# Optimization experiments

Hardware: AMD Instinct MI355X
Metric: run time of the kernel (lower is better)

The kernel has to match this reference:

```python
import jax, jax.numpy as jnp
import numpy as np
from jax import lax

D = 768
C = 37          # num_classes + 1
PAD_ID = C - 1  # label_init puts '[PAD]' last
B, S = 128, 512


def setup_inputs() -> dict:
    key = jax.random.key(0)
    ks = jax.random.split(key, 8)
    x = jax.random.normal(ks[0], (B, S, D), dtype=jnp.float32)
    W = jax.random.normal(ks[1], (D, C), dtype=jnp.float32) * (1.0 / np.sqrt(D))
    b = jnp.zeros((C,), dtype=jnp.float32)
    start = jax.random.uniform(ks[2], (C,), minval=-0.1, maxval=0.1)
    end = jax.random.uniform(ks[3], (C,), minval=-0.1, maxval=0.1)
    trans = jax.random.uniform(ks[4], (C, C), minval=-0.1, maxval=0.1)
    labels = jax.random.randint(ks[5], (B, S), 0, C)
    lengths = jax.random.randint(ks[6], (B,), 16, S + 1)
    mask = (jnp.arange(S)[None, :] < lengths[:, None])  # first column always True
    return {"x": x, "W": W, "b": b, "start": start, "end": end,
            "trans": trans, "labels": labels, "mask": mask}


def _crf(emissions, labels, mask, start, end, trans):
    # time-major, as in pytorch-crf
    em = jnp.transpose(emissions, (1, 0, 2))      # [S, B, C]
    tg = labels.T                                  # [S, B]
    mkb = mask.T                                   # [S, B] bool
    mkf = mkb.astype(em.dtype)
    bidx = jnp.arange(em.shape[1])

    # ---- gold path score ----
    score0 = start[tg[0]] + em[0, bidx, tg[0]]
    def step_score(carry, inp):
        prev_tag, s = carry
        e_t, t_t, mf, mb = inp
        s = s + (trans[prev_tag, t_t] + e_t[bidx, t_t]) * mf
        prev_tag = jnp.where(mb, t_t, prev_tag)
        return (prev_tag, s), None
    (last_tag, score), _ = lax.scan(step_score, (tg[0], score0),
                                    (em[1:], tg[1:], mkf[1:], mkb[1:]))
    score = score + end[last_tag]

    # ---- log partition (forward algorithm) ----
    alpha0 = start[None, :] + em[0]               # [B, C]
    def step_norm(alpha, inp):
        e_t, mb = inp
        nxt = jax.nn.logsumexp(alpha[:, :, None] + trans[None, :, :], axis=1) + e_t
        return jnp.where(mb[:, None], nxt, alpha), None
    alpha, _ = lax.scan(step_norm, alpha0, (em[1:], mkb[1:]))
    logZ = jax.nn.logsumexp(alpha + end[None, :], axis=1)
    ll = jnp.sum(score - logZ)                    # reduction='sum'

    # ---- Viterbi decode ----
    ident = jnp.arange(C)[None, :]
    v0 = start[None, :] + em[0]
    def step_vit(v, inp):
        e_t, mb = inp
        cand = v[:, :, None] + trans[None, :, :]  # [B, prev, cur]
        bp = jnp.argmax(cand, axis=1)             # [B, C]
        nxt = jnp.max(cand, axis=1) + e_t
        v = jnp.where(mb[:, None], nxt, v)
        bp = jnp.where(mb[:, None], bp, ident)    # identity at padded steps
        return v, bp
    v, bps = lax.scan(step_vit, v0, (em[1:], mkb[1:]))  # bps: [S-1, B, C]
    last = jnp.argmax(v + end[None, :], axis=1)   # [B]
    def back(tag, bp):
        return bp[bidx, tag], tag
    first, rest = lax.scan(back, last, bps, reverse=True)
    tags = jnp.concatenate([first[None, :], rest], axis=0).T  # [B, S]
    tags = jnp.where(mask, tags, PAD_ID)
    return ll, tags


def reference(x, W, b, start, end, trans, labels, mask):
    emissions = jnp.einsum('bsd,dc->bsc', x, W) + b  # linear head
    log_likelihood, tags = _crf(emissions, labels, mask, start, end, trans)
    return log_likelihood, tags
```

## Files before the change

### kernel.cpp

```cpp
#include <hip/hip_runtime.h>

#define Bq 128
#define Sq 512
#define Cq 37
#define Dq 768

typedef __attribute__((ext_vector_type(2))) float f32x2;
typedef __attribute__((ext_vector_type(4))) float f32x4;
typedef __attribute__((ext_vector_type(8))) short bf16x8;

static __device__ __forceinline__ f32x2 pk_fma(f32x2 a, f32x2 b, f32x2 c) {
  f32x2 d; asm("v_pk_fma_f32 %0, %1, %2, %3" : "=v"(d) : "v"(a), "v"(b), "v"(c));
  return d;
}
static __device__ __forceinline__ f32x2 pk_add(f32x2 a, f32x2 b) {
  f32x2 d; asm("v_pk_add_f32 %0, %1, %2" : "=v"(d) : "v"(a), "v"(b));
  return d;
}
static __device__ __forceinline__ float bcast(float v, int p) {
  return __int_as_float(__builtin_amdgcn_ds_bpermute(p << 2, __float_as_int(v)));
}

#define REP18(X) X(0)X(1)X(2)X(3)X(4)X(5)X(6)X(7)X(8)X(9)X(10)X(11)X(12)X(13) \
  X(14)X(15)X(16)X(17)
#define REP37(X) X(0)X(1)X(2)X(3)X(4)X(5)X(6)X(7)X(8)X(9)X(10)X(11)X(12)X(13) \
  X(14)X(15)X(16)X(17)X(18)X(19)X(20)X(21)X(22)X(23)X(24)X(25)X(26)X(27)X(28) \
  X(29)X(30)X(31)X(32)X(33)X(34)X(35)X(36)

__global__ __launch_bounds__(256) void prep_kernel(
    const float* __restrict__ W, unsigned short* __restrict__ Wbh,
    unsigned short* __restrict__ Wbl)
{
  int i = blockIdx.x * 256 + threadIdx.x;
  if (i >= 24 * 3 * 64 * 8) return;
  int ks = i / 1536, rem = i % 1536;
  int nt = rem / 512, rem2 = rem % 512;
  int lane = rem2 >> 3, j = rem2 & 7;
  int k = ks * 32 + (lane >> 4) * 8 + j;
  int c = nt * 16 + (lane & 15);
  float w = (c < Cq) ? W[(size_t)k * Cq + c] : 0.f;
  unsigned u = __float_as_uint(w);
  unsigned short h = (unsigned short)(u >> 16);
  float hr = __uint_as_float((unsigned)h << 16);
  float r = w - hr;
  Wbh[i] = h;
  Wbl[i] = (unsigned short)(__float_as_uint(r) >> 16);
}

__global__ __launch_bounds__(256) void emis_kernel(
    const float* __restrict__ x, const unsigned short* __restrict__ Wbh,
    const unsigned short* __restrict__ Wbl, const float* __restrict__ bias,
    float* __restrict__ em)
{
  int tid = threadIdx.x, lane = tid & 63;
  int wv = tid >> 6;
  int tokBase = blockIdx.x * 64 + wv * 16;
  int row = lane & 15, kg = lane >> 4;
  const float* xr = x + (size_t)(tokBase + row) * Dq + kg * 8;
  const bf16x8* Bh = (const bf16x8*)Wbh;
  const bf16x8* Bl = (const bf16x8*)Wbl;
  f32x4 acc0 = {0.f, 0.f, 0.f, 0.f};
  f32x4 acc1 = {0.f, 0.f, 0.f, 0.f};
  f32x4 acc2 = {0.f, 0.f, 0.f, 0.f};

  float4 c0 = *(const float4*)(xr);
  float4 c1 = *(const float4*)(xr + 4);
  for (int ks = 0; ks < 24; ++ks) {
    float4 n0, n1;
    if (ks < 23) {
      n0 = *(const float4*)(xr + (ks + 1) * 32);
      n1 = *(const float4*)(xr + (ks + 1) * 32 + 4);
    }
    bf16x8 ah, al;
#define SPLIT(J, V) { unsigned u = __float_as_uint(V); \
    unsigned short h = (unsigned short)(u >> 16); \
    float hr = __uint_as_float((unsigned)h << 16); \
    float rr = (V) - hr; \
    ah[J] = (short)h; al[J] = (short)(__float_as_uint(rr) >> 16); }
    SPLIT(0, c0.x) SPLIT(1, c0.y) SPLIT(2, c0.z) SPLIT(3, c0.w)
    SPLIT(4, c1.x) SPLIT(5, c1.y) SPLIT(6, c1.z) SPLIT(7, c1.w)
#undef SPLIT
    int fi = (ks * 3) * 64 + lane;
    bf16x8 bh0 = Bh[fi], bh1 = Bh[fi + 64], bh2 = Bh[fi + 128];
    bf16x8 bl0 = Bl[fi], bl1 = Bl[fi + 64], bl2 = Bl[fi + 128];
    acc0 = __builtin_amdgcn_mfma_f32_16x16x32_bf16(al, bh0, acc0, 0, 0, 0);
    acc1 = __builtin_amdgcn_mfma_f32_16x16x32_bf16(al, bh1, acc1, 0, 0, 0);
    acc2 = __builtin_amdgcn_mfma_f32_16x16x32_bf16(al, bh2, acc2, 0, 0, 0);
    acc0 = __builtin_amdgcn_mfma_f32_16x16x32_bf16(ah, bl0, acc0, 0, 0, 0);
    acc1 = __builtin_amdgcn_mfma_f32_16x16x32_bf16(ah, bl1, acc1, 0, 0, 0);
    acc2 = __builtin_amdgcn_mfma_f32_16x16x32_bf16(ah, bl2, acc2, 0, 0, 0);
    acc0 = __builtin_amdgcn_mfma_f32_16x16x32_bf16(ah, bh0, acc0, 0, 0, 0);
    acc1 = __builtin_amdgcn_mfma_f32_16x16x32_bf16(ah, bh1, acc1, 0, 0, 0);
    acc2 = __builtin_amdgcn_mfma_f32_16x16x32_bf16(ah, bh2, acc2, 0, 0, 0);
    c0 = n0; c1 = n1;
  }
  int colc = lane & 15;
#pragma unroll
  for (int r = 0; r < 4; ++r) {
    size_t tok = (size_t)tokBase + kg * 4 + r;
    em[tok * Cq + colc]      = acc0[r] + bias[colc];
    em[tok * Cq + 16 + colc] = acc1[r] + bias[16 + colc];
    if (colc < 5)
      em[tok * Cq + 32 + colc] = acc2[r] + bias[32 + colc];
  }
}

__global__ __launch_bounds__(320) void crf_mega_kernel(
    const float* __restrict__ em, const float* __restrict__ startv,
    const float* __restrict__ endv, const float* __restrict__ trans,
    const int* __restrict__ labels, const unsigned char* __restrict__ maskb,
    float* __restrict__ llp, float* __restrict__ outp)
{
  __shared__ float semm[(Sq + 4) * Cq];
  __shared__ float vh[Sq * 40];
  __shared__ __align__(16) float sxA[64];
  __shared__ __align__(16) float sxB[64];
  __shared__ __align__(16) float sxC[64];
  __shared__ __align__(16) float sxD[64];
  __shared__ float mrgA[64], mrgB[64], mrgV[64], mrgU[64];
  __shared__ float s_score;
  __shared__ int s_cstar;
  int b = blockIdx.x;
  int tid = threadIdx.x, wid = tid >> 6, lane = tid & 63;
  int cl = lane < Cq ? lane : Cq - 1;

  int esz4 = (maskb[1] == 0) ? 1 : 0;
  int len = 0;
#pragma unroll
  for (int k = 0; k < 8; ++k) {
    size_t t = (size_t)lane + (size_t)k * 64;
    unsigned char mb = esz4 ? maskb[((size_t)b * Sq + t) * 4] : maskb[(size_t)b * Sq + t];
    len += (mb != 0);
  }
#pragma unroll
  for (int off = 32; off; off >>= 1) len += __shfl_xor(len, off);
  int m = len >> 1;

  const float4* src4 = (const float4*)(em + (size_t)b * Sq * Cq);
  float4* dst4 = (float4*)semm;
  for (int i = tid; i < (Sq * Cq) / 4; i += 320) dst4[i] = src4[i];
  if (tid < 4 * Cq) semm[Sq * Cq + tid] = 0.f;
  __syncthreads();

  const float L2E = 1.4426950408889634f, LN2 = 0.6931471805599453f;

  if (wid == 0) {
    f32x2 E2[18];
#pragma unroll
    for (int i = 0; i < 18; ++i) {
      E2[i][0] = exp2f(trans[(2 * i) * Cq + cl] * L2E);
      E2[i][1] = exp2f(trans[(2 * i + 1) * Cq + cl] * L2E);
    }
    float E36 = exp2f(trans[36 * Cq + cl] * L2E);
    const float4* se4 = (const float4*)sxA;
    float a0 = (lane < Cq) ? (startv[cl] + semm[cl]) : -3.0e38f;
    float K0 = bcast(a0, 0);
    float ez = (lane < Cq) ? exp2f((a0 - K0) * L2E) : 0.f;
    int eacc = 0;
    float wA = exp2f(semm[1 * Cq + cl] * L2E), wB = exp2f(semm[2 * Cq + cl] * L2E);
    float wC = exp2f(semm[3 * Cq + cl] * L2E), wD = exp2f(semm[4 * Cq + cl] * L2E);
    for (int t = 1; t <= m; ++t) {
      sxA[lane] = ez;
      int tn = (t + 4 <= m) ? t + 4 : m;
      float raw = semm[tn * Cq + cl];
      float4 gv[10];
#pragma unroll
      for (int q = 0; q < 10; ++q) gv[q] = se4[q];
      int e0 = ((__float_as_int(gv[0].x) >> 23) & 255) - 127;
      float scale = __int_as_float((127 - e0) << 23);
      f32x2 sa = {0.f, 0.f}, sb2 = {0.f, 0.f};
#define FPK(i) { f32x2 g; \
      g[0] = ((i) & 1) ? gv[(i) >> 1].z : gv[(i) >> 1].x; \
      g[1] = ((i) & 1) ? gv[(i) >> 1].w : gv[(i) >> 1].y; \
      if ((i) & 1) sb2 = pk_fma(g, E2[i], sb2); else sa = pk_fma(g, E2[i], sa); }
      REP18(FPK)
#undef FPK
      float dot = ((sa[0] + sb2[0]) + (sa[1] + sb2[1])) + gv[9].x * E36;
      float wcur = wA; wA = wB; wB = wC; wC = wD;
      ez = dot * (wcur * scale);
      eacc += e0;
      wD = exp2f(raw * L2E);
    }
    mrgA[lane] = (lane < Cq) ? LN2 * (log2f(ez) + (float)eacc) + K0 : -3.0e38f;
  } else if (wid == 1) {
    f32x2 E2[18];
#pragma unroll
    for (int i = 0; i < 18; ++i) {
      E2[i][0] = exp2f(trans[cl * Cq + 2 * i] * L2E);
      E2[i][1] = exp2f(trans[cl * Cq + 2 * i + 1] * L2E);
    }
    float E36 = exp2f(trans[cl * Cq + 36] * L2E);
    const float4* se4 = (const float4*)sxB;
    float b0v = (lane < Cq) ? endv[cl] : -3.0e38f;
    float KB = bcast(b0v, 0);
    float bz = (lane < Cq) ? exp2f((b0v - KB) * L2E) : 0.f;
    int eacc = 0;
    float wA = exp2f(semm[(len - 1) * Cq + cl] * L2E);
    float wB = exp2f(semm[(len - 2) * Cq + cl] * L2E);
    float wC = exp2f(semm[(len - 3) * Cq + cl] * L2E);
    float wD = exp2f(semm[(len - 4) * Cq + cl] * L2E);
    for (int t = len - 2; t >= m; --t) {
      float wcur = wA; wA = wB; wB = wC; wC = wD;
      float s = bz * wcur;
      sxB[lane] = s;
      int tn = (t - 3 > 0) ? t - 3 : 0;
      float raw = semm[tn * Cq + cl];
      float4 gv[10];
#pragma unroll
      for (int q = 0; q < 10; ++q) gv[q] = se4[q];
      int e0 = ((__float_as_int(gv[0].x) >> 23) & 255) - 127;
      float scale = __int_as_float((127 - e0) << 23);
      f32x2 sa = {0.f, 0.f}, sb2 = {0.f, 0.f};
#define FPK(i) { f32x2 g; \
      g[0] = ((i) & 1) ? gv[(i) >> 1].z : gv[(i) >> 1].x; \
      g[1] = ((i) & 1) ? gv[(i) >> 1].w : gv[(i) >> 1].y; \
      if ((i) & 1) sb2 = pk_fma(g, E2[i], sb2); else sa = pk_fma(g, E2[i], sa); }
      REP18(FPK)
#undef FPK
      float dot = ((sa[0] + sb2[0]) + (sa[1] + sb2[1])) + gv[9].x * E36;
      bz = dot * scale;
      eacc += e0;
      wD = exp2f(raw * L2E);
    }
    mrgB[lane] = (lane < Cq) ? LN2 * (log2f(bz) + (float)eacc) + KB : -3.0e38f;
  } else if (wid == 2) {
    f32x2 T2[18];
#pragma unroll
    for (int i = 0; i < 18; ++i) {
      T2[i][0] = trans[(2 * i) * Cq + cl];
      T2[i][1] = trans[(2 * i + 1) * Cq + cl];
    }
    float T36 = trans[36 * Cq + cl];
    const float4* sv4 = (const float4*)sxC;
    float v = (lane < Cq) ? (startv[cl] + semm[cl]) : -3.0e38f;
    vh[0 * 40 + lane] = (lane < Cq) ? v : -3.0e38f;
    float emA = semm[1 * Cq + cl], emB = semm[2 * Cq + cl];
    float emC = semm[3 * Cq + cl], emD = semm[4 * Cq + cl];
    for (int t = 1; t <= m; ++t) {
      sxC[lane] = v;
      int tn = (t + 4 <= m) ? t + 4 : m;
      float raw = semm[tn * Cq + cl];
      float4 gv[10];
#pragma unroll
      for (int q = 0; q < 10; ++q) gv[q] = sv4[q];
      float m0 = -3.0e38f, m1 = -3.0e38f, m2 = -3.0e38f, m3 = -3.0e38f;
#define VPK(i) { f32x2 g; \
      g[0] = ((i) & 1) ? gv[(i) >> 1].z : gv[(i) >> 1].x; \
      g[1] = ((i) & 1) ? gv[(i) >> 1].w : gv[(i) >> 1].y; \
      f32x2 c = pk_add(g, T2[i]); \
      if (((i) & 3) == 0) m0 = fmaxf(fmaxf(m0, c[0]), c[1]); \
      else if (((i) & 3) == 1) m1 = fmaxf(fmaxf(m1, c[0]), c[1]); \
      else if (((i) & 3) == 2) m2 = fmaxf(fmaxf(m2, c[0]), c[1]); \
      else m3 = fmaxf(fmaxf(m3, c[0]), c[1]); }
      REP18(VPK)
#undef VPK
      float c36 = gv[9].x + T36;
      float best = fmaxf(fmaxf(fmaxf(m0, m1), fmaxf(m2, m3)), c36);
      float emc = emA; emA = emB; emB = emC; emC = emD;
      v = (lane < Cq) ? best + emc : -3.0e38f;
      vh[t * 40 + lane] = v;
      emD = raw;
    }
    mrgV[lane] = v;
  } else if (wid == 3) {
    f32x2 T2[18];
#pragma unroll
    for (int i = 0; i < 18; ++i) {
      T2[i][0] = trans[cl * Cq + 2 * i];
      T2[i][1] = trans[cl * Cq + 2 * i + 1];
    }
    float T36 = trans[cl * Cq + 36];
    const float4* sv4 = (const float4*)sxD;
    float u = (lane < Cq) ? endv[cl] : -3.0e38f;
    float emA = semm[(len - 1) * Cq + cl], emB = semm[(len - 2) * Cq + cl];
    float emC = semm[(len - 3) * Cq + cl], emD = semm[(len - 4) * Cq + cl];
    for (int t = len - 2; t >= m; --t) {
      float emc = emA; emA = emB; emB = emC; emC = emD;
      float s = u + emc;
      sxD[lane] = s;
      vh[(t + 1) * 40 + lane] = (lane < Cq) ? s : -3.0e38f;
      int tn = (t - 3 > 0) ? t - 3 : 0;
      float raw = semm[tn * Cq + cl];
      float4 gv[10];
#pragma unroll
      for (int q = 0; q < 10; ++q) gv[q] = sv4[q];
      float m0 = -3.0e38f, m1 = -3.0e38f, m2 = -3.0e38f, m3 = -3.0e38f;
#define VPK(i) { f32x2 g; \
      g[0] = ((i) & 1) ? gv[(i) >> 1].z : gv[(i) >> 1].x; \
      g[1] = ((i) & 1) ? gv[(i) >> 1].w : gv[(i) >> 1].y; \
      f32x2 c = pk_add(g, T2[i]); \
      if (((i) & 3) == 0) m0 = fmaxf(fmaxf(m0, c[0]), c[1]); \
      else if (((i) & 3) == 1) m1 = fmaxf(fmaxf(m1, c[0]), c[1]); \
      else if (((i) & 3) == 2) m2 = fmaxf(fmaxf(m2, c[0]), c[1]); \
      else m3 = fmaxf(fmaxf(m3, c[0]), c[1]); }
      REP18(VPK)
#undef VPK
      float c36 = gv[9].x + T36;
      float best = fmaxf(fmaxf(fmaxf(m0, m1), fmaxf(m2, m3)), c36);
      u = (lane < Cq) ? best : -3.0e38f;
      emD = raw;
    }
    mrgU[lane] = u;
  } else {
    const int* lab = labels + (size_t)b * Sq;
    float sc = 0.f;
#pragma unroll
    for (int k = 0; k < 8; ++k) {
      int t = 1 + lane + k * 64;
      if (t < len) {
        int lp = lab[t - 1], lt = lab[t];
        sc += trans[lp * Cq + lt] + semm[t * Cq + lt];
      }
    }
#pragma unroll
    for (int off = 32; off; off >>= 1) sc += __shfl_xor(sc, off);
    if (lane == 0) {
      int l0 = lab[0], lf = lab[len - 1];
      s_score = sc + startv[l0] + semm[l0] + endv[lf];
    }
  }
  __syncthreads();

  unsigned char* bpl = (unsigned char*)semm;
  if (wid == 0) {
    float xv = (lane < Cq) ? mrgA[lane] + mrgB[lane] : -3.0e38f;
    float mm = xv;
#pragma unroll
    for (int off = 32; off; off >>= 1) mm = fmaxf(mm, __shfl_xor(mm, off));
    float es = exp2f((xv - mm) * L2E);
#pragma unroll
    for (int off = 32; off; off >>= 1) es += __shfl_xor(es, off);
    float logZ = mm + log2f(es) * LN2;
    float pv = (lane < Cq) ? mrgV[lane] + mrgU[lane] : -3.0e38f;
    int idx = (lane < Cq) ? lane : 1000;
#pragma unroll
    for (int off = 32; off; off >>= 1) {
      float po = __shfl_xor(pv, off); int io = __shfl_xor(idx, off);
      if (po > pv || (po == pv && io < idx)) { pv = po; idx = io; }
    }
    if (lane == 0) { llp[b] = s_score - logZ; s_cstar = idx; }
  } else if (wid <= 2) {
#define DECLT(i) float T##i = trans[(i) * Cq + cl];
    REP37(DECLT)
#undef DECLT
    for (int t = wid; t <= m; t += 2) {
      const float4* vr4 = (const float4*)&vh[(t - 1) * 40];
      float4 gv[10];
#pragma unroll
      for (int q = 0; q < 10; ++q) gv[q] = vr4[q];
      float br[40]; float4* br4 = (float4*)br;
#pragma unroll
      for (int q = 0; q < 10; ++q) br4[q] = gv[q];
      float best = -3.0e38f; int bi = 0;
#define BARG(i) { float cnd = br[i] + T##i; if (cnd > best) { best = cnd; bi = (i); } }
      REP37(BARG)
#undef BARG
      if (lane < Cq) bpl[cl * 520 + t] = (unsigned char)bi;
    }
  } else {
#define DECLR(i) float R##i = trans[cl * Cq + (i)];
    REP37(DECLR)
#undef DECLR
    for (int s = m + 1 + (wid - 3); s < len; s += 2) {
      const float4* vr4 = (const float4*)&vh[s * 40];
      float4 gv[10];
#pragma unroll
      for (int q = 0; q < 10; ++q) gv[q] = vr4[q];
      float br[40]; float4* br4 = (float4*)br;
#pragma unroll
      for (int q = 0; q < 10; ++q) br4[q] = gv[q];
      float best = -3.0e38f; int bi = 0;
#define BARG(i) { float cnd = br[i] + R##i; if (cnd > best) { best = cnd; bi = (i); } }
      REP37(BARG)
#undef BARG
      if (lane < Cq) bpl[cl * 520 + s] = (unsigned char)bi;
    }
  }
  __syncthreads();

  if (wid == 0) {
    int cstar = __builtin_amdgcn_readfirstlane(s_cstar);
    int lenv = __builtin_amdgcn_readfirstlane(len);
    int mv = __builtin_amdgcn_readfirstlane(m);
    int rowc = lane < Cq ? lane : Cq - 1;
    const unsigned* rw = (const unsigned*)(bpl + rowc * 520);
    unsigned r[128];
#pragma unroll
    for (int k = 0; k < 128; ++k) r[k] = rw[k];
    unsigned vt[8];
#pragma unroll
    for (int j = 0; j < 8; ++j) vt[j] = 0u;
#pragma unroll
    for (int j = 0; j < 8; ++j)
      vt[j] = (lane == (mv & 63) && (mv >> 6) == j) ? (unsigned)cstar : vt[j];
    {
      int tag = cstar;
#pragma unroll
      for (int t = 1; t <= 510; ++t) {
        int word = __builtin_amdgcn_readlane((int)r[t >> 2], tag);
        int nt = (word >> ((t & 3) * 8)) & 0xff;
        bool live = (t > mv) && (t < lenv);
        tag = live ? nt : tag;
        vt[t >> 6] = (lane == (t & 63) && live) ? (unsigned)tag : vt[t >> 6];
      }
    }
    {
      int tag = cstar;
#pragma unroll
      for (int t = 510; t >= 0; --t) {
        int word = __builtin_amdgcn_readlane((int)r[(t + 1) >> 2], tag);
        int nt = (word >> (((t + 1) & 3) * 8)) & 0xff;
        bool live = (t + 1 <= mv);
        tag = live ? nt : tag;
        vt[t >> 6] = (lane == (t & 63) && live) ? (unsigned)tag : vt[t >> 6];
      }
    }
#pragma unroll
    for (int j = 0; j < 8; ++j) {
      int t = j * 64 + lane;
      float o = (t < lenv) ? (float)(int)vt[j] : 36.0f;
      outp[(size_t)b * Sq + t] = o;
    }
  }
}

__global__ __launch_bounds__(64) void ll_reduce_kernel(
    const float* __restrict__ llp, float* __restrict__ outp)
{
  int lane = threadIdx.x;
  float s = llp[lane] + llp[lane + 64];
#pragma unroll
  for (int off = 32; off; off >>= 1) s += __shfl_xor(s, off);
  if (lane == 0) outp[0] = s;
}

extern "C" void kernel_launch(void* const* d_in, const int* in_sizes, int n_in,
                              void* d_out, int out_size, void* d_ws, size_t ws_size,
                              hipStream_t stream)
{
  const float* x      = (const float*)d_in[0];
  const float* W      = (const float*)d_in[1];
  const float* bias   = (const float*)d_in[2];
  const float* startv = (const float*)d_in[3];
  const float* endv   = (const float*)d_in[4];
  const float* trans  = (const float*)d_in[5];
  const int*   labels = (const int*)d_in[6];
  const unsigned char* maskb = (const unsigned char*)d_in[7];
  float* out = (float*)d_out;

  char* ws = (char*)d_ws;
  float* em            = (float*)(ws);
  float* llp           = (float*)(ws + 9699328);
  unsigned short* Wbh  = (unsigned short*)(ws + 9699840);
  unsigned short* Wbl  = (unsigned short*)(ws + 9773568);

  prep_kernel<<<144, 256, 0, stream>>>(W, Wbh, Wbl);
  emis_kernel<<<1024, 256, 0, stream>>>(x, Wbh, Wbl, bias, em);
  crf_mega_kernel<<<128, 320, 0, stream>>>(em, startv, endv, trans, labels, maskb,
                                           llp, out + 1);
  ll_reduce_kernel<<<1, 64, 0, stream>>>(llp, out);
}
```

Measured before the change: 187.3 us.

## Balance backpointer argmax across all waves and split traceback into two waves

The backpointer computation, previously split between two fixed wave pairs (forward and backward halves), now runs on all five waves with interleaved rows. Each argmax is done as a tree-based max followed by a min-index reduction instead of a serial compare chain. The forward and backward Viterbi traceback chains move onto separate waves so they run concurrently, and each wave writes only its own part of the output. The intent is to shorten the serial tail of the decode phase. The cost is higher register pressure from holding both transition vectors and all candidates, and tie-breaking now relies on exact equality with the max.

```diff
diff --git a/kernel.cpp b/kernel.cpp
--- a/kernel.cpp
+++ b/kernel.cpp
@@ -20,12 +20,16 @@
 static __device__ __forceinline__ float bcast(float v, int p) {
   return __int_as_float(__builtin_amdgcn_ds_bpermute(p << 2, __float_as_int(v)));
 }
+static __device__ __forceinline__ int imin(int a, int b) { return a < b ? a : b; }
 
 #define REP18(X) X(0)X(1)X(2)X(3)X(4)X(5)X(6)X(7)X(8)X(9)X(10)X(11)X(12)X(13) \
   X(14)X(15)X(16)X(17)
 #define REP37(X) X(0)X(1)X(2)X(3)X(4)X(5)X(6)X(7)X(8)X(9)X(10)X(11)X(12)X(13) \
   X(14)X(15)X(16)X(17)X(18)X(19)X(20)X(21)X(22)X(23)X(24)X(25)X(26)X(27)X(28) \
   X(29)X(30)X(31)X(32)X(33)X(34)X(35)X(36)
+
+#define BR(i) ((((i) & 3) == 0) ? gv[(i) >> 2].x : (((i) & 3) == 1) ? gv[(i) >> 2].y \
+             : (((i) & 3) == 2) ? gv[(i) >> 2].z : gv[(i) >> 2].w)
 
 __global__ __launch_bounds__(256) void prep_kernel(
     const float* __restrict__ W, unsigned short* __restrict__ Wbh,
@@ -233,7 +237,7 @@
     float T36 = trans[36 * Cq + cl];
     const float4* sv4 = (const float4*)sxC;
     float v = (lane < Cq) ? (startv[cl] + semm[cl]) : -3.0e38f;
-    vh[0 * 40 + lane] = (lane < Cq) ? v : -3.0e38f;
+    if (lane < 40) vh[0 * 40 + lane] = v;
     float emA = semm[1 * Cq + cl], emB = semm[2 * Cq + cl];
     float emC = semm[3 * Cq + cl], emD = semm[4 * Cq + cl];
     for (int t = 1; t <= m; ++t) {
@@ -258,7 +262,7 @@
       float best = fmaxf(fmaxf(fmaxf(m0, m1), fmaxf(m2, m3)), c36);
       float emc = emA; emA = emB; emB = emC; emC = emD;
       v = (lane < Cq) ? best + emc : -3.0e38f;
-      vh[t * 40 + lane] = v;
+      if (lane < 40) vh[t * 40 + lane] = v;
       emD = raw;
     }
     mrgV[lane] = v;
@@ -278,7 +282,7 @@
       float emc = emA; emA = emB; emB = emC; emC = emD;
       float s = u + emc;
       sxD[lane] = s;
-      vh[(t + 1) * 40 + lane] = (lane < Cq) ? s : -3.0e38f;
+      if (lane < 40) vh[(t + 1) * 40 + lane] = (lane < Cq) ? s : -3.0e38f;
       int tn = (t - 3 > 0) ? t - 3 : 0;
       float raw = semm[tn * Cq + cl];
       float4 gv[10];
@@ -339,46 +343,78 @@
       if (po > pv || (po == pv && io < idx)) { pv = po; idx = io; }
     }
     if (lane == 0) { llp[b] = s_score - logZ; s_cstar = idx; }
-  } else if (wid <= 2) {
-#define DECLT(i) float T##i = trans[(i) * Cq + cl];
-    REP37(DECLT)
-#undef DECLT
-    for (int t = wid; t <= m; t += 2) {
-      const float4* vr4 = (const float4*)&vh[(t - 1) * 40];
+  }
+  {
+#define DT(i) float T##i = trans[(i) * Cq + cl];
+    REP37(DT)
+#undef DT
+#define DR(i) float R##i = trans[cl * Cq + (i)];
+    REP37(DR)
+#undef DR
+    for (int r = 1 + wid; r < len; r += 5) {
+      int isbp = (r <= m);
+      const float4* vr4 = (const float4*)&vh[(isbp ? r - 1 : r) * 40];
       float4 gv[10];
 #pragma unroll
       for (int q = 0; q < 10; ++q) gv[q] = vr4[q];
-      float br[40]; float4* br4 = (float4*)br;
-#pragma unroll
-      for (int q = 0; q < 10; ++q) br4[q] = gv[q];
-      float best = -3.0e38f; int bi = 0;
-#define BARG(i) { float cnd = br[i] + T##i; if (cnd > best) { best = cnd; bi = (i); } }
-      REP37(BARG)
-#undef BARG
-      if (lane < Cq) bpl[cl * 520 + t] = (unsigned char)bi;
-    }
-  } else {
-#define DECLR(i) float R##i = trans[cl * Cq + (i)];
-    REP37(DECLR)
-#undef DECLR
-    for (int s = m + 1 + (wid - 3); s < len; s += 2) {
-      const float4* vr4 = (const float4*)&vh[s * 40];
-      float4 gv[10];
-#pragma unroll
-      for (int q = 0; q < 10; ++q) gv[q] = vr4[q];
-      float br[40]; float4* br4 = (float4*)br;
-#pragma unroll
-      for (int q = 0; q < 10; ++q) br4[q] = gv[q];
-      float best = -3.0e38f; int bi = 0;
-#define BARG(i) { float cnd = br[i] + R##i; if (cnd > best) { best = cnd; bi = (i); } }
-      REP37(BARG)
-#undef BARG
-      if (lane < Cq) bpl[cl * 520 + s] = (unsigned char)bi;
+      int bi;
+      if (isbp) {
+#define CNDT(i) float C##i = BR(i) + T##i;
+        REP37(CNDT)
+#undef CNDT
+        float b0 = fmaxf(fmaxf(C0, C1), C2),   b1 = fmaxf(fmaxf(C3, C4), C5);
+        float b2 = fmaxf(fmaxf(C6, C7), C8),   b3 = fmaxf(fmaxf(C9, C10), C11);
+        float b4 = fmaxf(fmaxf(C12, C13), C14), b5 = fmaxf(fmaxf(C15, C16), C17);
+        float b6 = fmaxf(fmaxf(C18, C19), C20), b7 = fmaxf(fmaxf(C21, C22), C23);
+        float b8 = fmaxf(fmaxf(C24, C25), C26), b9 = fmaxf(fmaxf(C27, C28), C29);
+        float b10 = fmaxf(fmaxf(C30, C31), C32), b11 = fmaxf(fmaxf(C33, C34), C35);
+        float c0 = fmaxf(fmaxf(b0, b1), b2), c1 = fmaxf(fmaxf(b3, b4), b5);
+        float c2 = fmaxf(fmaxf(b6, b7), b8), c3 = fmaxf(fmaxf(b9, b10), b11);
+        float best = fmaxf(fmaxf(fmaxf(c0, c1), fmaxf(c2, c3)), C36);
+#define IDX(i) int I##i = (C##i == best) ? (i) : 63;
+        REP37(IDX)
+#undef IDX
+        int d0 = imin(imin(I0, I1), I2),   d1 = imin(imin(I3, I4), I5);
+        int d2 = imin(imin(I6, I7), I8),   d3 = imin(imin(I9, I10), I11);
+        int d4 = imin(imin(I12, I13), I14), d5 = imin(imin(I15, I16), I17);
+        int d6 = imin(imin(I18, I19), I20), d7 = imin(imin(I21, I22), I23);
+        int d8 = imin(imin(I24, I25), I26), d9 = imin(imin(I27, I28), I29);
+        int d10 = imin(imin(I30, I31), I32), d11 = imin(imin(I33, I34), I35);
+        int e0i = imin(imin(d0, d1), d2), e1i = imin(imin(d3, d4), d5);
+        int e2i = imin(imin(d6, d7), d8), e3i = imin(imin(d9, d10), d11);
+        bi = imin(imin(imin(e0i, e1i), imin(e2i, e3i)), I36);
+      } else {
+#define CNDR(i) float C##i = BR(i) + R##i;
+        REP37(CNDR)
+#undef CNDR
+        float b0 = fmaxf(fmaxf(C0, C1), C2),   b1 = fmaxf(fmaxf(C3, C4), C5);
+        float b2 = fmaxf(fmaxf(C6, C7), C8),   b3 = fmaxf(fmaxf(C9, C10), C11);
+        float b4 = fmaxf(fmaxf(C12, C13), C14), b5 = fmaxf(fmaxf(C15, C16), C17);
+        float b6 = fmaxf(fmaxf(C18, C19), C20), b7 = fmaxf(fmaxf(C21, C22), C23);
+        float b8 = fmaxf(fmaxf(C24, C25), C26), b9 = fmaxf(fmaxf(C27, C28), C29);
+        float b10 = fmaxf(fmaxf(C30, C31), C32), b11 = fmaxf(fmaxf(C33, C34), C35);
+        float c0 = fmaxf(fmaxf(b0, b1), b2), c1 = fmaxf(fmaxf(b3, b4), b5);
+        float c2 = fmaxf(fmaxf(b6, b7), b8), c3 = fmaxf(fmaxf(b9, b10), b11);
+        float best = fmaxf(fmaxf(fmaxf(c0, c1), fmaxf(c2, c3)), C36);
+#define IDX(i) int I##i = (C##i == best) ? (i) : 63;
+        REP37(IDX)
+#undef IDX
+        int d0 = imin(imin(I0, I1), I2),   d1 = imin(imin(I3, I4), I5);
+        int d2 = imin(imin(I6, I7), I8),   d3 = imin(imin(I9, I10), I11);
+        int d4 = imin(imin(I12, I13), I14), d5 = imin(imin(I15, I16), I17);
+        int d6 = imin(imin(I18, I19), I20), d7 = imin(imin(I21, I22), I23);
+        int d8 = imin(imin(I24, I25), I26), d9 = imin(imin(I27, I28), I29);
+        int d10 = imin(imin(I30, I31), I32), d11 = imin(imin(I33, I34), I35);
+        int e0i = imin(imin(d0, d1), d2), e1i = imin(imin(d3, d4), d5);
+        int e2i = imin(imin(d6, d7), d8), e3i = imin(imin(d9, d10), d11);
+        bi = imin(imin(imin(e0i, e1i), imin(e2i, e3i)), I36);
+      }
+      if (lane < Cq) bpl[cl * 520 + r] = (unsigned char)bi;
     }
   }
   __syncthreads();
 
-  if (wid == 0) {
+  if (wid <= 1) {
     int cstar = __builtin_amdgcn_readfirstlane(s_cstar);
     int lenv = __builtin_amdgcn_readfirstlane(len);
     int mv = __builtin_amdgcn_readfirstlane(m);
@@ -390,10 +426,25 @@
     unsigned vt[8];
 #pragma unroll
     for (int j = 0; j < 8; ++j) vt[j] = 0u;
-#pragma unroll
-    for (int j = 0; j < 8; ++j)
-      vt[j] = (lane == (mv & 63) && (mv >> 6) == j) ? (unsigned)cstar : vt[j];
-    {
+    if (wid == 0) {
+#pragma unroll
+      for (int j = 0; j < 8; ++j)
+        vt[j] = (lane == (mv & 63) && (mv >> 6) == j) ? (unsigned)cstar : vt[j];
+      int tag = cstar;
+#pragma unroll
+      for (int t = 510; t >= 0; --t) {
+        int word = __builtin_amdgcn_readlane((int)r[(t + 1) >> 2], tag);
+        int nt = (word >> (((t + 1) & 3) * 8)) & 0xff;
+        bool live = (t + 1 <= mv);
+        tag = live ? nt : tag;
+        vt[t >> 6] = (lane == (t & 63) && live) ? (unsigned)tag : vt[t >> 6];
+      }
+#pragma unroll
+      for (int j = 0; j < 8; ++j) {
+        int t = j * 64 + lane;
+        if (t <= mv) outp[(size_t)b * Sq + t] = (float)(int)vt[j];
+      }
+    } else {
       int tag = cstar;
 #pragma unroll
       for (int t = 1; t <= 510; ++t) {
@@ -403,23 +454,14 @@
         tag = live ? nt : tag;
         vt[t >> 6] = (lane == (t & 63) && live) ? (unsigned)tag : vt[t >> 6];
       }
-    }
-    {
-      int tag = cstar;
-#pragma unroll
-      for (int t = 510; t >= 0; --t) {
-        int word = __builtin_amdgcn_readlane((int)r[(t + 1) >> 2], tag);
-        int nt = (word >> (((t + 1) & 3) * 8)) & 0xff;
-        bool live = (t + 1 <= mv);
-        tag = live ? nt : tag;
-        vt[t >> 6] = (lane == (t & 63) && live) ? (unsigned)tag : vt[t >> 6];
+#pragma unroll
+      for (int j = 0; j < 8; ++j) {
+        int t = j * 64 + lane;
+        if (t > mv) {
+          float o = (t < lenv) ? (float)(int)vt[j] : 36.0f;
+          outp[(size_t)b * Sq + t] = o;
+        }
       }
-    }
-#pragma unroll
-    for (int j = 0; j < 8; ++j) {
-      int t = j * 64 + lane;
-      float o = (t < lenv) ? (float)(int)vt[j] : 36.0f;
-      outp[(size_t)b * Sq + t] = o;
     }
   }
 }
```

New measurement: 215.9 us. 15.3% more time.

## Split Viterbi backtrace across two waves and stream backpointer rows in chunks

Applied to the files above, without the earlier changes.

The backtrace previously ran serially in one wave, walking forward from the midpoint and then backward to the start. It now assigns each half to a separate wave so the two run concurrently. Each wave loads backpointer words in 16-word chunks instead of holding 128 registers, and uses ds_bpermute for the tag lookup in place of readlane. The change also drops the register copy into a br array in the argmax loops and limits vh stores to lanes below 40. Risks are the higher latency of bpermute on the dependent chain and the two waves writing disjoint output ranges.

```diff
diff --git a/kernel.cpp b/kernel.cpp
--- a/kernel.cpp
+++ b/kernel.cpp
@@ -26,6 +26,9 @@
 #define REP37(X) X(0)X(1)X(2)X(3)X(4)X(5)X(6)X(7)X(8)X(9)X(10)X(11)X(12)X(13) \
   X(14)X(15)X(16)X(17)X(18)X(19)X(20)X(21)X(22)X(23)X(24)X(25)X(26)X(27)X(28) \
   X(29)X(30)X(31)X(32)X(33)X(34)X(35)X(36)
+
+#define BR(i) ((((i) & 3) == 0) ? gv[(i) >> 2].x : (((i) & 3) == 1) ? gv[(i) >> 2].y \
+             : (((i) & 3) == 2) ? gv[(i) >> 2].z : gv[(i) >> 2].w)
 
 __global__ __launch_bounds__(256) void prep_kernel(
     const float* __restrict__ W, unsigned short* __restrict__ Wbh,
@@ -233,7 +236,7 @@
     float T36 = trans[36 * Cq + cl];
     const float4* sv4 = (const float4*)sxC;
     float v = (lane < Cq) ? (startv[cl] + semm[cl]) : -3.0e38f;
-    vh[0 * 40 + lane] = (lane < Cq) ? v : -3.0e38f;
+    if (lane < 40) vh[0 * 40 + lane] = v;
     float emA = semm[1 * Cq + cl], emB = semm[2 * Cq + cl];
     float emC = semm[3 * Cq + cl], emD = semm[4 * Cq + cl];
     for (int t = 1; t <= m; ++t) {
@@ -258,7 +261,7 @@
       float best = fmaxf(fmaxf(fmaxf(m0, m1), fmaxf(m2, m3)), c36);
       float emc = emA; emA = emB; emB = emC; emC = emD;
       v = (lane < Cq) ? best + emc : -3.0e38f;
-      vh[t * 40 + lane] = v;
+      if (lane < 40) vh[t * 40 + lane] = v;
       emD = raw;
     }
     mrgV[lane] = v;
@@ -278,7 +281,7 @@
       float emc = emA; emA = emB; emB = emC; emC = emD;
       float s = u + emc;
       sxD[lane] = s;
-      vh[(t + 1) * 40 + lane] = (lane < Cq) ? s : -3.0e38f;
+      if (lane < 40) vh[(t + 1) * 40 + lane] = (lane < Cq) ? s : -3.0e38f;
       int tn = (t - 3 > 0) ? t - 3 : 0;
       float raw = semm[tn * Cq + cl];
       float4 gv[10];
@@ -340,37 +343,31 @@
     }
     if (lane == 0) { llp[b] = s_score - logZ; s_cstar = idx; }
   } else if (wid <= 2) {
-#define DECLT(i) float T##i = trans[(i) * Cq + cl];
-    REP37(DECLT)
-#undef DECLT
+#define DT(i) float T##i = trans[(i) * Cq + cl];
+    REP37(DT)
+#undef DT
     for (int t = wid; t <= m; t += 2) {
       const float4* vr4 = (const float4*)&vh[(t - 1) * 40];
       float4 gv[10];
 #pragma unroll
       for (int q = 0; q < 10; ++q) gv[q] = vr4[q];
-      float br[40]; float4* br4 = (float4*)br;
-#pragma unroll
-      for (int q = 0; q < 10; ++q) br4[q] = gv[q];
       float best = -3.0e38f; int bi = 0;
-#define BARG(i) { float cnd = br[i] + T##i; if (cnd > best) { best = cnd; bi = (i); } }
+#define BARG(i) { float cnd = BR(i) + T##i; if (cnd > best) { best = cnd; bi = (i); } }
       REP37(BARG)
 #undef BARG
       if (lane < Cq) bpl[cl * 520 + t] = (unsigned char)bi;
     }
   } else {
-#define DECLR(i) float R##i = trans[cl * Cq + (i)];
-    REP37(DECLR)
-#undef DECLR
+#define DR(i) float R##i = trans[cl * Cq + (i)];
+    REP37(DR)
+#undef DR
     for (int s = m + 1 + (wid - 3); s < len; s += 2) {
       const float4* vr4 = (const float4*)&vh[s * 40];
       float4 gv[10];
 #pragma unroll
       for (int q = 0; q < 10; ++q) gv[q] = vr4[q];
-      float br[40]; float4* br4 = (float4*)br;
-#pragma unroll
-      for (int q = 0; q < 10; ++q) br4[q] = gv[q];
       float best = -3.0e38f; int bi = 0;
-#define BARG(i) { float cnd = br[i] + R##i; if (cnd > best) { best = cnd; bi = (i); } }
+#define BARG(i) { float cnd = BR(i) + R##i; if (cnd > best) { best = cnd; bi = (i); } }
       REP37(BARG)
 #undef BARG
       if (lane < Cq) bpl[cl * 520 + s] = (unsigned char)bi;
@@ -378,48 +375,67 @@
   }
   __syncthreads();
 
-  if (wid == 0) {
+  if (wid <= 1) {
     int cstar = __builtin_amdgcn_readfirstlane(s_cstar);
     int lenv = __builtin_amdgcn_readfirstlane(len);
     int mv = __builtin_amdgcn_readfirstlane(m);
     int rowc = lane < Cq ? lane : Cq - 1;
     const unsigned* rw = (const unsigned*)(bpl + rowc * 520);
-    unsigned r[128];
-#pragma unroll
-    for (int k = 0; k < 128; ++k) r[k] = rw[k];
     unsigned vt[8];
 #pragma unroll
     for (int j = 0; j < 8; ++j) vt[j] = 0u;
-#pragma unroll
-    for (int j = 0; j < 8; ++j)
-      vt[j] = (lane == (mv & 63) && (mv >> 6) == j) ? (unsigned)cstar : vt[j];
-    {
-      int tag = cstar;
-#pragma unroll
-      for (int t = 1; t <= 510; ++t) {
-        int word = __builtin_amdgcn_readlane((int)r[t >> 2], tag);
-        int nt = (word >> ((t & 3) * 8)) & 0xff;
-        bool live = (t > mv) && (t < lenv);
-        tag = live ? nt : tag;
-        vt[t >> 6] = (lane == (t & 63) && live) ? (unsigned)tag : vt[t >> 6];
+    int tag = cstar;
+    if (wid == 0) {
+#pragma unroll
+      for (int j = 0; j < 8; ++j)
+        vt[j] = (lane == (mv & 63) && (mv >> 6) == j) ? (unsigned)cstar : vt[j];
+#pragma unroll
+      for (int k = 7; k >= 0; --k) {
+        unsigned rc[16];
+#pragma unroll
+        for (int w = 0; w < 16; ++w) rc[w] = rw[16 * k + w];
+#pragma unroll
+        for (int tt = 63; tt >= 0; --tt) {
+          int p = 64 * k + tt;
+          if (p == 0) continue;
+          int t = p - 1;
+          int word = __builtin_amdgcn_ds_bpermute(tag << 2, (int)rc[tt >> 2]);
+          int nt = (word >> ((tt & 3) * 8)) & 0xff;
+          bool live = (p <= mv);
+          tag = live ? nt : tag;
+          vt[t >> 6] = (lane == (t & 63) && live) ? (unsigned)tag : vt[t >> 6];
+        }
       }
-    }
-    {
-      int tag = cstar;
-#pragma unroll
-      for (int t = 510; t >= 0; --t) {
-        int word = __builtin_amdgcn_readlane((int)r[(t + 1) >> 2], tag);
-        int nt = (word >> (((t + 1) & 3) * 8)) & 0xff;
-        bool live = (t + 1 <= mv);
-        tag = live ? nt : tag;
-        vt[t >> 6] = (lane == (t & 63) && live) ? (unsigned)tag : vt[t >> 6];
+#pragma unroll
+      for (int j = 0; j < 8; ++j) {
+        int t = j * 64 + lane;
+        if (t <= mv) outp[(size_t)b * Sq + t] = (float)(int)vt[j];
       }
-    }
-#pragma unroll
-    for (int j = 0; j < 8; ++j) {
-      int t = j * 64 + lane;
-      float o = (t < lenv) ? (float)(int)vt[j] : 36.0f;
-      outp[(size_t)b * Sq + t] = o;
+    } else {
+#pragma unroll
+      for (int k = 0; k < 8; ++k) {
+        unsigned rc[16];
+#pragma unroll
+        for (int w = 0; w < 16; ++w) rc[w] = rw[16 * k + w];
+#pragma unroll
+        for (int tt = 0; tt < 64; ++tt) {
+          int t = 64 * k + tt;
+          if (t == 0) continue;
+          int word = __builtin_amdgcn_ds_bpermute(tag << 2, (int)rc[tt >> 2]);
+          int nt = (word >> ((tt & 3) * 8)) & 0xff;
+          bool live = (t > mv) && (t < lenv);
+          tag = live ? nt : tag;
+          vt[t >> 6] = (lane == (t & 63) && live) ? (unsigned)tag : vt[t >> 6];
+        }
+      }
+#pragma unroll
+      for (int j = 0; j < 8; ++j) {
+        int t = j * 64 + lane;
+        if (t > mv) {
+          float o = (t < lenv) ? (float)(int)vt[j] : 36.0f;
+          outp[(size_t)b * Sq + t] = o;
+        }
+      }
     }
   }
 }
```

New measurement: 236.4 us. 26.2% more time.
